# Performance work log

Hardware: AMD Instinct MI355X
Metric: run time of the kernel (lower is better)

## Reference

```python
import jax, jax.numpy as jnp
import numpy as np

MASK_FILL = -1e-07  # faithful to original (tiny negative, not -1e7)


def setup_inputs() -> dict:
    key = jax.random.key(0)
    k1, k2, k3, k4 = jax.random.split(key, 4)
    B, L1, L2, D = 64, 1024, 1024, 256
    v1 = jax.random.normal(k1, (B, L1, D), dtype=jnp.float32)
    v2 = jax.random.normal(k2, (B, L2, D), dtype=jnp.float32)
    v1_mask = jax.random.randint(k3, (B, L1), 0, 2).astype(bool)  # True = pad
    v2_mask = jax.random.randint(k4, (B, L2), 0, 2).astype(bool)
    return {"v1": v1, "v1_mask": v1_mask, "v2": v2, "v2_mask": v2_mask}


def reference(v1, v1_mask, v2, v2_mask):
    # sim: [B, L1, L2]
    sim = jnp.einsum('bld,bmd->blm', v1, v2)
    # mask rows (pad positions of v1), then softmax over L1 (dim=1)
    sim1 = jnp.where(v1_mask[:, :, None], MASK_FILL, sim)
    v2_v1_attn = jax.nn.softmax(sim1, axis=1)
    # mask columns on the already row-masked matrix, softmax over L2 (dim=2)
    sim2 = jnp.where(v2_mask[:, None, :], MASK_FILL, sim1)
    v1_v2_attn = jax.nn.softmax(sim2, axis=2)
    attended_v1 = jnp.einsum('blm,bmd->bld', v1_v2_attn, v2)  # [B, L1, D]
    attended_v2 = jnp.einsum('blm,bld->bmd', v2_v1_attn, v1)  # [B, L2, D]
    attended_v1 = jnp.where(v1_mask[:, :, None], 0.0, attended_v1)
    attended_v2 = jnp.where(v2_mask[:, :, None], 0.0, attended_v2)
    return attended_v1, attended_v2
```

## Files before the change

kernel.cpp:

```cpp
#include <hip/hip_runtime.h>
#include <hip/hip_bf16.h>
#include <hip/hip_fp16.h>
#include <stdint.h>


#define MASK_FILL -1e-07f

typedef unsigned short u16;
typedef _Float16 half8 __attribute__((ext_vector_type(8)));
typedef __attribute__((ext_vector_type(4))) float f32x4;
typedef __attribute__((ext_vector_type(4))) u16 u16x4;

#define NB 64
#define LL 1024
#define DD 256
#define BQ 128
#define HB 32
#define ELEMS ((size_t)NB * LL * DD)
#define NIT_STREAM 128

__device__ __forceinline__ u16 f16b(float f) {
    _Float16 h = (_Float16)f;
    return __builtin_bit_cast(u16, h);
}
__device__ __forceinline__ unsigned pkf16(float a, float b) {
    return (unsigned)f16b(a) | ((unsigned)f16b(b) << 16);
}

__device__ __forceinline__ void gll16(const u16* g, u16* l) {
    __builtin_amdgcn_global_load_lds(
        (const __attribute__((address_space(1))) void*)g,
        (__attribute__((address_space(3))) void*)l, 16, 0, 0);
}

__global__ __launch_bounds__(256) void prep_masks(
    const void* __restrict__ m1, const void* __restrict__ m2,
    int* __restrict__ cm1, int* __restrict__ cm2,
    int* __restrict__ qidx1, int* __restrict__ pa1, int* __restrict__ qcnt1,
    int* __restrict__ qidx2, int* __restrict__ pa2, int* __restrict__ qcnt2,
    int* __restrict__ ctr)
{
    int blk = blockIdx.x, tid = threadIdx.x;
    int msk = blk >> 6, b = blk & 63;
    const unsigned* w1 = (const unsigned*)m1;
    const unsigned* w2 = (const unsigned*)m2;
    unsigned acc = 0;
    for (int i = tid; i < 4096; i += 256) acc |= (w1[i] | w2[i]) & ~1u;
    __shared__ unsigned red[256];
    red[tid] = acc;
    __syncthreads();
    for (int o = 128; o; o >>= 1) {
        if (tid < o) red[tid] |= red[tid + o];
        __syncthreads();
    }
    int isbool = red[0] ? 1 : 0;

    const void* m = msk ? m2 : m1;
    int* cm   = msk ? cm2 : cm1;
    int* qidx = msk ? qidx2 : qidx1;
    int* pa   = msk ? pa2 : pa1;
    int* qcnt = msk ? qcnt2 : qcnt1;

    __shared__ int ps[256];
    int f[4], s = 0;
#pragma unroll
    for (int j = 0; j < 4; ++j) {
        int idx = b * LL + tid * 4 + j;
        int v = isbool ? (int)((const unsigned char*)m)[idx] : ((const int*)m)[idx];
        cm[idx] = v ? 1 : 0;
        f[j] = (v == 0) ? 1 : 0;
        s += f[j];
    }
    ps[tid] = s;
    __syncthreads();
    for (int off = 1; off < 256; off <<= 1) {
        int v = (tid >= off) ? ps[tid - off] : 0;
        __syncthreads();
        ps[tid] += v;
        __syncthreads();
    }
    int pos = (tid > 0) ? ps[tid - 1] : 0;
#pragma unroll
    for (int j = 0; j < 4; ++j) {
        pa[b * LL + tid * 4 + j] = pos;
        if (f[j]) qidx[b * LL + (pos++)] = tid * 4 + j;
    }
    if (tid == 255) qcnt[b] = ps[255];
    if (blk == 0 && tid < 8) ctr[tid] = 0;
}

__global__ __launch_bounds__(256) void prep2_kernel(
    const float* __restrict__ x1, u16* __restrict__ h1, u16* __restrict__ t1,
    const int* __restrict__ cm1, const int* __restrict__ pa1,
    const int* __restrict__ qi1, const int* __restrict__ qc1,
    const float* __restrict__ x2, u16* __restrict__ h2, u16* __restrict__ t2,
    const int* __restrict__ cm2, const int* __restrict__ pa2,
    const int* __restrict__ qi2, const int* __restrict__ qc2,
    float* __restrict__ part, float* __restrict__ out)
{
    __shared__ u16 t[64][65];
    __shared__ float ps2[16][68];
    int blk = blockIdx.x;
    int tensor = blk >> 12;
    blk &= 4095;
    const float* x = tensor ? x2 : x1;
    u16* h  = tensor ? h2 : h1;
    u16* xt = tensor ? t2 : t1;
    const int* cm = tensor ? cm2 : cm1;
    const int* pa = tensor ? pa2 : pa1;
    const int* qi = tensor ? qi2 : qi1;
    const int* qc = tensor ? qc2 : qc1;
    float* outb = out + (tensor ? ELEMS : 0);
    int b = blk >> 6, lt = (blk >> 2) & 15, dt = blk & 3;
    int l0 = lt * 64, d0 = dt * 64;
    int tid = threadIdx.x;
    int sub = tid >> 4;
    int c16 = tid & 15;
    float vpart[4] = {0.f, 0.f, 0.f, 0.f};
#pragma unroll
    for (int p = 0; p < 4; ++p) {
        int row = p * 16 + sub;
        int l = l0 + row;
        int masked = cm[b * LL + l];
        int slot = pa[b * LL + l];
        f32x4 v = *(const f32x4*)(x + ((size_t)b * LL + l) * DD + d0 + c16 * 4);
        u16x4 hv;
#pragma unroll
        for (int e = 0; e < 4; ++e) {
            hv[e] = f16b(v[e]);
            t[c16 * 4 + e][row] = hv[e];
            if (masked) vpart[e] += v[e];
        }
        if (!masked) {
            *(u16x4*)(h + ((size_t)b * LL + slot) * DD + d0 + c16 * 4) = hv;
        } else {
            f32x4 z4 = {0.f, 0.f, 0.f, 0.f};
            *(f32x4*)(outb + ((size_t)b * LL + l) * DD + d0 + c16 * 4) = z4;
        }
    }
#pragma unroll
    for (int e = 0; e < 4; ++e) ps2[sub][c16 * 4 + e] = vpart[e];
    __syncthreads();
    int first = pa[b * LL + l0];
    int cntb = qc[b];
    int nun = ((lt == 15) ? cntb : pa[b * LL + l0 + 64]) - first;
    int last = first + nun;
    int q0 = first >> 2;
    int nq = ((last + 3) >> 2) - q0;
    const int* qib = qi + b * LL;
#pragma unroll
    for (int p = 0; p < 4; ++p) {
        int d = p * 16 + sub;
        u16* xrow = xt + ((size_t)b * DD + d0 + d) * LL;
        for (int qq = c16; qq < nq; qq += 16) {
            int s0 = (q0 + qq) << 2;
            if (s0 >= first && s0 + 4 <= last) {
                u16x4 ov;
#pragma unroll
                for (int e = 0; e < 4; ++e) {
                    int col = qib[s0 + e] - l0;
                    ov[e] = t[d][col];
                }
                *(u16x4*)(xrow + s0) = ov;
            } else {
#pragma unroll
                for (int e = 0; e < 4; ++e) {
                    int sl = s0 + e;
                    if (sl >= first && sl < last) {
                        int col = qib[sl] - l0;
                        xrow[sl] = t[d][col];
                    }
                }
            }
        }
    }
    if (tid < 64) {
        float s = 0.f;
#pragma unroll
        for (int k = 0; k < 16; ++k) s += ps2[k][tid];
        part[(((size_t)tensor * NB + b) * 16 + lt) * 256 + d0 + tid] = s;
    }
}

__global__ __launch_bounds__(256) void vsum_reduce(
    const float* __restrict__ part, float* __restrict__ vsum)
{
    int blk = blockIdx.x;
    int d = threadIdx.x;
    float s = 0.f;
#pragma unroll
    for (int lt = 0; lt < 16; ++lt)
        s += part[((size_t)blk * 16 + lt) * 256 + d];
    vsum[(size_t)blk * DD + d] = s;
}

__global__ __launch_bounds__(512, 2) void flash_fused(
    const u16* __restrict__ v1h, const u16* __restrict__ v2h,
    const u16* __restrict__ v1t, const u16* __restrict__ v2t,
    const int* __restrict__ qidx1, const int* __restrict__ qcnt1,
    const int* __restrict__ qidx2, const int* __restrict__ qcnt2,
    const float* __restrict__ vsum, int* __restrict__ ctr,
    float* __restrict__ out)
{
    int strm0 = blockIdx.x & 7;
    int tid = threadIdx.x;
    int w = tid >> 6, lane = tid & 63;
    int lq = lane & 15, g = lane >> 4;

    __shared__ __align__(16) u16 khs[2][2][HB * DD];
    __shared__ __align__(16) u16 vts[2][2][HB * DD];

    const int pvcc = (g ^ (lq & 3) ^ ((lq >> 2) & 3)) * 8;

#define STAGE(BUF, KT2)                                                         \
    {                                                                           \
        int k0s = (KT2) * 64;                                                   \
        _Pragma("unroll")                                                       \
        for (int t = 0; t < 8; ++t) {                                           \
            int u = t * 8 + w;                                                  \
            int n = u & 15;                                                     \
            int hh = (u >> 4) & 1;                                              \
            if (u < 32) {                                                       \
                unsigned phys = (unsigned)n * 1024u + (unsigned)lane * 16u;     \
                unsigned key = phys >> 9;                                       \
                unsigned cl = ((phys >> 4) & 31u) ^ (key & 7u);                 \
                size_t koff = kv_base + (size_t)(k0s + hh * HB + (int)key) * DD + cl * 8; \
                gll16(kh_g + koff, &khs[BUF][hh][n * 512]);                     \
            } else {                                                            \
                unsigned dv = (unsigned)n * 16u + ((unsigned)lane >> 2);        \
                unsigned cv = ((unsigned)lane & 3u) ^ (dv & 3u) ^ ((dv >> 2) & 3u); \
                size_t voff = vt_base + (size_t)dv * LL + (unsigned)(k0s + hh * HB) + cv * 8; \
                gll16(vt_g + voff, &vts[BUF][hh][n * 512]);                     \
            }                                                                   \
        }                                                                       \
    }

    for (int ss = 0; ss < 8; ++ss) {
        int s2 = (strm0 + ss) & 7;
        for (;;) {
            __syncthreads();
            if (tid == 0) *(int*)&khs[0][0][0] = atomicAdd(&ctr[s2], 1);
            __syncthreads();
            int it = *(const int*)&khs[0][0][0];
            __syncthreads();
            if (it >= NIT_STREAM) break;
            int qt  = it & 7;
            int dir = (it >> 3) & 1;
            int b   = ((it >> 4) << 3) + s2;

            const u16 *qh_g, *kh_g, *vt_g;
            const int *qidx, *qcq, *qck;
            const float* vsp;
            float* ob;
            if (dir == 0) { qh_g=v1h; kh_g=v2h; vt_g=v2t;
                            qidx=qidx1; qcq=qcnt1; qck=qcnt2;
                            vsp = vsum + ((size_t)NB + b) * DD; ob = out; }
            else          { qh_g=v2h; kh_g=v1h; vt_g=v1t;
                            qidx=qidx2; qcq=qcnt2; qck=qcnt1;
                            vsp = vsum + (size_t)b * DD; ob = out + ELEMS; }
            int cnt_q = qcq[b];
            if (qt * BQ >= cnt_q) continue;
            int cnt_k = qck[b];
            int nkt2 = (cnt_k + 63) >> 6;

            int qslot = qt * BQ + w * 16 + lq;
            bool qvalid = qslot < cnt_q;

            const u16* qbh = qh_g + ((size_t)b * LL + qslot) * DD + g * 8;
            half8 qhf[8];
#pragma unroll
            for (int ks = 0; ks < 8; ++ks)
                qhf[ks] = *(const half8*)(const void*)(qbh + ks * 32);

            float m = MASK_FILL, z = 0.f;
            f32x4 o[16];
#pragma unroll
            for (int i2 = 0; i2 < 16; ++i2) o[i2] = (f32x4){0.f, 0.f, 0.f, 0.f};

            const size_t kv_base = (size_t)b * LL * DD;
            const size_t vt_base = (size_t)b * DD * LL;

            if (nkt2 > 0) {
                int cur = 0;
                STAGE(0, 0);
                asm volatile("s_waitcnt vmcnt(0)" ::: "memory");
                __builtin_amdgcn_s_barrier();
                __builtin_amdgcn_sched_barrier(0);

                for (int kt2 = 0; kt2 < nkt2; ++kt2) {
                    int k0 = kt2 * 64;
                    if (kt2 + 1 < nkt2) STAGE(cur ^ 1, kt2 + 1);

                    f32x4 sa[2][2];
#pragma unroll
                    for (int hh = 0; hh < 2; ++hh)
#pragma unroll
                        for (int rt = 0; rt < 2; ++rt)
                            sa[hh][rt] = (f32x4){0.f, 0.f, 0.f, 0.f};
                    __builtin_amdgcn_s_setprio(1);
#pragma unroll
                    for (int hh = 0; hh < 2; ++hh) {
#pragma unroll
                        for (int ks = 0; ks < 8; ++ks) {
                            int cidx = ((ks * 4 + g) ^ (lq & 7)) * 8;
                            half8 kh0 = *(const half8*)(const void*)&khs[cur][hh][lq * 256 + cidx];
                            half8 kh1 = *(const half8*)(const void*)&khs[cur][hh][(16 + lq) * 256 + cidx];
                            sa[hh][0] = __builtin_amdgcn_mfma_f32_16x16x32_f16(kh0, qhf[ks], sa[hh][0], 0, 0, 0);
                            sa[hh][1] = __builtin_amdgcn_mfma_f32_16x16x32_f16(kh1, qhf[ks], sa[hh][1], 0, 0, 0);
                        }
                    }
                    __builtin_amdgcn_s_setprio(0);

                    half8 vfA[8], vfB[8];
#pragma unroll
                    for (int dt = 0; dt < 8; ++dt) {
                        int d = dt * 16 + lq;
                        vfA[dt] = *(const half8*)(const void*)&vts[cur][0][d * 32 + pvcc];
                        vfB[dt] = *(const half8*)(const void*)&vts[cur][1][d * 32 + pvcc];
                    }

                    float s[16];
#pragma unroll
                    for (int hh = 0; hh < 2; ++hh)
#pragma unroll
                        for (int i2 = 0; i2 < 4; ++i2) {
                            s[hh * 8 + i2]     = sa[hh][0][i2];
                            s[hh * 8 + 4 + i2] = sa[hh][1][i2];
                        }
                    if (kt2 == nkt2 - 1) {
#pragma unroll
                        for (int hh = 0; hh < 2; ++hh) {
                            int base = k0 + hh * HB + 4 * g;
#pragma unroll
                            for (int i2 = 0; i2 < 4; ++i2) {
                                if (base + i2 >= cnt_k)      s[hh * 8 + i2]     = -1e30f;
                                if (base + 16 + i2 >= cnt_k) s[hh * 8 + 4 + i2] = -1e30f;
                            }
                        }
                    }
                    float pmax = s[0];
#pragma unroll
                    for (int i2 = 1; i2 < 16; ++i2) pmax = fmaxf(pmax, s[i2]);
                    pmax = fmaxf(pmax, __shfl_xor(pmax, 16));
                    pmax = fmaxf(pmax, __shfl_xor(pmax, 32));
                    if (__any(pmax > m)) {
                        float mnew = fmaxf(m, pmax);
                        float alpha = __expf(m - mnew);
                        z *= alpha;
#pragma unroll
                        for (int i2 = 0; i2 < 16; ++i2) o[i2] *= alpha;
                        m = mnew;
                    }
                    float p[16], psum = 0.f;
#pragma unroll
                    for (int i2 = 0; i2 < 16; ++i2) { p[i2] = __expf(s[i2] - m); psum += p[i2]; }
                    psum += __shfl_xor(psum, 16);
                    psum += __shfl_xor(psum, 32);
                    z += psum;

                    union { unsigned u[4]; half8 v; } pf[2];
                    int srcA = ((lane & 16) << 1) | lq;
                    int srcB = srcA + 16;
                    bool sel = (g >> 1) != 0;
#pragma unroll
                    for (int hh = 0; hh < 2; ++hh) {
                        unsigned pk00 = pkf16(p[hh * 8 + 0], p[hh * 8 + 1]);
                        unsigned pk01 = pkf16(p[hh * 8 + 2], p[hh * 8 + 3]);
                        unsigned pk10 = pkf16(p[hh * 8 + 4], p[hh * 8 + 5]);
                        unsigned pk11 = pkf16(p[hh * 8 + 6], p[hh * 8 + 7]);
                        unsigned a00 = (unsigned)__shfl((int)pk00, srcA);
                        unsigned a01 = (unsigned)__shfl((int)pk01, srcA);
                        unsigned a10 = (unsigned)__shfl((int)pk10, srcA);
                        unsigned a11 = (unsigned)__shfl((int)pk11, srcA);
                        unsigned b00 = (unsigned)__shfl((int)pk00, srcB);
                        unsigned b01 = (unsigned)__shfl((int)pk01, srcB);
                        unsigned b10 = (unsigned)__shfl((int)pk10, srcB);
                        unsigned b11 = (unsigned)__shfl((int)pk11, srcB);
                        pf[hh].u[0] = sel ? a10 : a00;
                        pf[hh].u[1] = sel ? a11 : a01;
                        pf[hh].u[2] = sel ? b10 : b00;
                        pf[hh].u[3] = sel ? b11 : b01;
                    }

                    __builtin_amdgcn_s_setprio(1);
#pragma unroll
                    for (int dt = 0; dt < 8; ++dt) {
                        o[dt] = __builtin_amdgcn_mfma_f32_16x16x32_f16(vfA[dt], pf[0].v, o[dt], 0, 0, 0);
                        o[dt] = __builtin_amdgcn_mfma_f32_16x16x32_f16(vfB[dt], pf[1].v, o[dt], 0, 0, 0);
                    }
#pragma unroll
                    for (int dt = 8; dt < 16; ++dt) {
                        int d = dt * 16 + lq;
                        half8 vf0 = *(const half8*)(const void*)&vts[cur][0][d * 32 + pvcc];
                        half8 vf1 = *(const half8*)(const void*)&vts[cur][1][d * 32 + pvcc];
                        o[dt] = __builtin_amdgcn_mfma_f32_16x16x32_f16(vf0, pf[0].v, o[dt], 0, 0, 0);
                        o[dt] = __builtin_amdgcn_mfma_f32_16x16x32_f16(vf1, pf[1].v, o[dt], 0, 0, 0);
                    }
                    __builtin_amdgcn_s_setprio(0);

                    if (kt2 + 1 < nkt2) {
                        asm volatile("s_waitcnt vmcnt(0)" ::: "memory");
                        __builtin_amdgcn_s_barrier();
                        __builtin_amdgcn_sched_barrier(0);
                    }
                    cur ^= 1;
                }
            }

            float wl = __expf(MASK_FILL - m);
            z += (float)(LL - cnt_k) * wl;
#pragma unroll
            for (int dt = 0; dt < 16; ++dt) {
                f32x4 vv = *(const f32x4*)(vsp + dt * 16 + 4 * g);
                o[dt] += wl * vv;
            }

            if (qvalid) {
                int qrow = qidx[b * LL + qslot];
                float zinv = 1.0f / z;
                float* orow = ob + ((size_t)b * LL + qrow) * DD + 4 * g;
#pragma unroll
                for (int dt = 0; dt < 16; ++dt) {
                    f32x4 vv = o[dt] * zinv;
                    *(f32x4*)(orow + dt * 16) = vv;
                }
            }
        }
    }
#undef STAGE
}

extern "C" void kernel_launch(void* const* d_in, const int* in_sizes, int n_in,
                              void* d_out, int out_size, void* d_ws, size_t ws_size,
                              hipStream_t stream)
{
    const float* v1      = (const float*)d_in[0];
    const void*  v1_mask = d_in[1];
    const float* v2      = (const float*)d_in[2];
    const void*  v2_mask = d_in[3];
    float* out = (float*)d_out;

    u16* v1h = (u16*)d_ws;
    u16* v2h = v1h + ELEMS;
    u16* v1t = v2h + ELEMS;
    u16* v2t = v1t + ELEMS;
    int* qidx1 = (int*)(v2t + ELEMS);
    int* qcnt1 = qidx1 + NB * LL;
    int* qidx2 = qcnt1 + NB;
    int* qcnt2 = qidx2 + NB * LL;
    int* cm1   = qcnt2 + NB;
    int* cm2   = cm1 + NB * LL;
    int* pa1   = cm2 + NB * LL;
    int* pa2   = pa1 + NB * LL;
    int* ctr   = pa2 + NB * LL;
    float* part = (float*)(ctr + 16);
    float* vsum = part + 2 * NB * 16 * 256;

    prep_masks<<<dim3(128), dim3(256), 0, stream>>>(
        v1_mask, v2_mask, cm1, cm2,
        qidx1, pa1, qcnt1, qidx2, pa2, qcnt2, ctr);

    prep2_kernel<<<dim3(2 * NB * 64), dim3(256), 0, stream>>>(
        v1, v1h, v1t, cm1, pa1, qidx1, qcnt1,
        v2, v2h, v2t, cm2, pa2, qidx2, qcnt2, part, out);
    vsum_reduce<<<dim3(2 * NB), dim3(256), 0, stream>>>(part, vsum);

    flash_fused<<<dim3(256), dim3(512), 0, stream>>>(
        v1h, v2h, v1t, v2t,
        qidx1, qcnt1, qidx2, qcnt2, vsum, ctr, out);
}
```

Before: 208.6 us.

## Shrink query tile to 64 and key tile to 32 with 4-wave blocks

Halves the query tile per work item (4 waves, 256 threads) and processes a single 32-key half-tile per iteration instead of two. The grid doubles to 512 blocks and LDS per block drops to a quarter, so more blocks can fit per CU and the persistent work queue gets finer-grained items that balance better. In exchange, each K/V tile staged into LDS is reused by fewer query rows, and there are twice as many barrier-synchronised iterations, each with less MFMA work to hide load latency behind.

```diff
diff --git a/kernel.cpp b/kernel.cpp
--- a/kernel.cpp
+++ b/kernel.cpp
@@ -14,10 +14,10 @@
 #define NB 64
 #define LL 1024
 #define DD 256
-#define BQ 128
+#define BQ 64
 #define HB 32
 #define ELEMS ((size_t)NB * LL * DD)
-#define NIT_STREAM 128
+#define NIT_STREAM 256
 
 __device__ __forceinline__ u16 f16b(float f) {
     _Float16 h = (_Float16)f;
@@ -194,7 +194,7 @@
     vsum[(size_t)blk * DD + d] = s;
 }
 
-__global__ __launch_bounds__(512, 2) void flash_fused(
+__global__ __launch_bounds__(256, 2) void flash_fused(
     const u16* __restrict__ v1h, const u16* __restrict__ v2h,
     const u16* __restrict__ v1t, const u16* __restrict__ v2t,
     const int* __restrict__ qidx1, const int* __restrict__ qcnt1,
@@ -207,30 +207,29 @@
     int w = tid >> 6, lane = tid & 63;
     int lq = lane & 15, g = lane >> 4;
 
-    __shared__ __align__(16) u16 khs[2][2][HB * DD];
-    __shared__ __align__(16) u16 vts[2][2][HB * DD];
+    __shared__ __align__(16) u16 khs[2][HB * DD];
+    __shared__ __align__(16) u16 vts[2][HB * DD];
 
     const int pvcc = (g ^ (lq & 3) ^ ((lq >> 2) & 3)) * 8;
 
-#define STAGE(BUF, KT2)                                                         \
+#define STAGE(BUF, KT)                                                          \
     {                                                                           \
-        int k0s = (KT2) * 64;                                                   \
+        int k0s = (KT) * HB;                                                    \
         _Pragma("unroll")                                                       \
         for (int t = 0; t < 8; ++t) {                                           \
-            int u = t * 8 + w;                                                  \
+            int u = t * 4 + w;                                                  \
             int n = u & 15;                                                     \
-            int hh = (u >> 4) & 1;                                              \
-            if (u < 32) {                                                       \
+            if (u < 16) {                                                       \
                 unsigned phys = (unsigned)n * 1024u + (unsigned)lane * 16u;     \
                 unsigned key = phys >> 9;                                       \
                 unsigned cl = ((phys >> 4) & 31u) ^ (key & 7u);                 \
-                size_t koff = kv_base + (size_t)(k0s + hh * HB + (int)key) * DD + cl * 8; \
-                gll16(kh_g + koff, &khs[BUF][hh][n * 512]);                     \
+                size_t koff = kv_base + (size_t)(k0s + (int)key) * DD + cl * 8; \
+                gll16(kh_g + koff, &khs[BUF][n * 512]);                         \
             } else {                                                            \
                 unsigned dv = (unsigned)n * 16u + ((unsigned)lane >> 2);        \
                 unsigned cv = ((unsigned)lane & 3u) ^ (dv & 3u) ^ ((dv >> 2) & 3u); \
-                size_t voff = vt_base + (size_t)dv * LL + (unsigned)(k0s + hh * HB) + cv * 8; \
-                gll16(vt_g + voff, &vts[BUF][hh][n * 512]);                     \
+                size_t voff = vt_base + (size_t)dv * LL + (unsigned)k0s + cv * 8;   \
+                gll16(vt_g + voff, &vts[BUF][n * 512]);                         \
             }                                                                   \
         }                                                                       \
     }
@@ -239,14 +238,14 @@
         int s2 = (strm0 + ss) & 7;
         for (;;) {
             __syncthreads();
-            if (tid == 0) *(int*)&khs[0][0][0] = atomicAdd(&ctr[s2], 1);
+            if (tid == 0) *(int*)&khs[0][0] = atomicAdd(&ctr[s2], 1);
             __syncthreads();
-            int it = *(const int*)&khs[0][0][0];
+            int it = *(const int*)&khs[0][0];
             __syncthreads();
             if (it >= NIT_STREAM) break;
-            int qt  = it & 7;
-            int dir = (it >> 3) & 1;
-            int b   = ((it >> 4) << 3) + s2;
+            int qt  = it & 15;
+            int dir = (it >> 4) & 1;
+            int b   = ((it >> 5) << 3) + s2;
 
             const u16 *qh_g, *kh_g, *vt_g;
             const int *qidx, *qcq, *qck;
@@ -261,7 +260,7 @@
             int cnt_q = qcq[b];
             if (qt * BQ >= cnt_q) continue;
             int cnt_k = qck[b];
-            int nkt2 = (cnt_k + 63) >> 6;
+            int nkt = (cnt_k + HB - 1) >> 5;
 
             int qslot = qt * BQ + w * 16 + lq;
             bool qvalid = qslot < cnt_q;
@@ -280,67 +279,51 @@
             const size_t kv_base = (size_t)b * LL * DD;
             const size_t vt_base = (size_t)b * DD * LL;
 
-            if (nkt2 > 0) {
+            if (nkt > 0) {
                 int cur = 0;
                 STAGE(0, 0);
                 asm volatile("s_waitcnt vmcnt(0)" ::: "memory");
                 __builtin_amdgcn_s_barrier();
                 __builtin_amdgcn_sched_barrier(0);
 
-                for (int kt2 = 0; kt2 < nkt2; ++kt2) {
-                    int k0 = kt2 * 64;
-                    if (kt2 + 1 < nkt2) STAGE(cur ^ 1, kt2 + 1);
-
-                    f32x4 sa[2][2];
-#pragma unroll
-                    for (int hh = 0; hh < 2; ++hh)
-#pragma unroll
-                        for (int rt = 0; rt < 2; ++rt)
-                            sa[hh][rt] = (f32x4){0.f, 0.f, 0.f, 0.f};
+                for (int kt = 0; kt < nkt; ++kt) {
+                    int k0 = kt * HB;
+                    if (kt + 1 < nkt) STAGE(cur ^ 1, kt + 1);
+
+                    f32x4 sa0 = (f32x4){0.f, 0.f, 0.f, 0.f};
+                    f32x4 sa1 = (f32x4){0.f, 0.f, 0.f, 0.f};
                     __builtin_amdgcn_s_setprio(1);
 #pragma unroll
-                    for (int hh = 0; hh < 2; ++hh) {
-#pragma unroll
-                        for (int ks = 0; ks < 8; ++ks) {
-                            int cidx = ((ks * 4 + g) ^ (lq & 7)) * 8;
-                            half8 kh0 = *(const half8*)(const void*)&khs[cur][hh][lq * 256 + cidx];
-                            half8 kh1 = *(const half8*)(const void*)&khs[cur][hh][(16 + lq) * 256 + cidx];
-                            sa[hh][0] = __builtin_amdgcn_mfma_f32_16x16x32_f16(kh0, qhf[ks], sa[hh][0], 0, 0, 0);
-                            sa[hh][1] = __builtin_amdgcn_mfma_f32_16x16x32_f16(kh1, qhf[ks], sa[hh][1], 0, 0, 0);
-                        }
+                    for (int ks = 0; ks < 8; ++ks) {
+                        int cidx = ((ks * 4 + g) ^ (lq & 7)) * 8;
+                        half8 kh0 = *(const half8*)(const void*)&khs[cur][lq * 256 + cidx];
+                        half8 kh1 = *(const half8*)(const void*)&khs[cur][(16 + lq) * 256 + cidx];
+                        sa0 = __builtin_amdgcn_mfma_f32_16x16x32_f16(kh0, qhf[ks], sa0, 0, 0, 0);
+                        sa1 = __builtin_amdgcn_mfma_f32_16x16x32_f16(kh1, qhf[ks], sa1, 0, 0, 0);
                     }
                     __builtin_amdgcn_s_setprio(0);
 
-                    half8 vfA[8], vfB[8];
+                    half8 vf[8];
 #pragma unroll
                     for (int dt = 0; dt < 8; ++dt) {
                         int d = dt * 16 + lq;
-                        vfA[dt] = *(const half8*)(const void*)&vts[cur][0][d * 32 + pvcc];
-                        vfB[dt] = *(const half8*)(const void*)&vts[cur][1][d * 32 + pvcc];
-                    }
-
-                    float s[16];
-#pragma unroll
-                    for (int hh = 0; hh < 2; ++hh)
+                        vf[dt] = *(const half8*)(const void*)&vts[cur][d * 32 + pvcc];
+                    }
+
+                    float s[8];
+#pragma unroll
+                    for (int i2 = 0; i2 < 4; ++i2) { s[i2] = sa0[i2]; s[4 + i2] = sa1[i2]; }
+                    if (kt == nkt - 1) {
+                        int base = k0 + 4 * g;
 #pragma unroll
                         for (int i2 = 0; i2 < 4; ++i2) {
-                            s[hh * 8 + i2]     = sa[hh][0][i2];
-                            s[hh * 8 + 4 + i2] = sa[hh][1][i2];
+                            if (base + i2 >= cnt_k)      s[i2]     = -1e30f;
+                            if (base + 16 + i2 >= cnt_k) s[4 + i2] = -1e30f;
                         }
-                    if (kt2 == nkt2 - 1) {
-#pragma unroll
-                        for (int hh = 0; hh < 2; ++hh) {
-                            int base = k0 + hh * HB + 4 * g;
-#pragma unroll
-                            for (int i2 = 0; i2 < 4; ++i2) {
-                                if (base + i2 >= cnt_k)      s[hh * 8 + i2]     = -1e30f;
-                                if (base + 16 + i2 >= cnt_k) s[hh * 8 + 4 + i2] = -1e30f;
-                            }
-                        }
                     }
                     float pmax = s[0];
 #pragma unroll
-                    for (int i2 = 1; i2 < 16; ++i2) pmax = fmaxf(pmax, s[i2]);
+                    for (int i2 = 1; i2 < 8; ++i2) pmax = fmaxf(pmax, s[i2]);
                     pmax = fmaxf(pmax, __shfl_xor(pmax, 16));
                     pmax = fmaxf(pmax, __shfl_xor(pmax, 32));
                     if (__any(pmax > m)) {
@@ -351,54 +334,47 @@
                         for (int i2 = 0; i2 < 16; ++i2) o[i2] *= alpha;
                         m = mnew;
                     }
-                    float p[16], psum = 0.f;
-#pragma unroll
-                    for (int i2 = 0; i2 < 16; ++i2) { p[i2] = __expf(s[i2] - m); psum += p[i2]; }
+                    float p[8], psum = 0.f;
+#pragma unroll
+                    for (int i2 = 0; i2 < 8; ++i2) { p[i2] = __expf(s[i2] - m); psum += p[i2]; }
                     psum += __shfl_xor(psum, 16);
                     psum += __shfl_xor(psum, 32);
                     z += psum;
 
-                    union { unsigned u[4]; half8 v; } pf[2];
+                    unsigned pk00 = pkf16(p[0], p[1]);
+                    unsigned pk01 = pkf16(p[2], p[3]);
+                    unsigned pk10 = pkf16(p[4], p[5]);
+                    unsigned pk11 = pkf16(p[6], p[7]);
                     int srcA = ((lane & 16) << 1) | lq;
                     int srcB = srcA + 16;
+                    unsigned a00 = (unsigned)__shfl((int)pk00, srcA);
+                    unsigned a01 = (unsigned)__shfl((int)pk01, srcA);
+                    unsigned a10 = (unsigned)__shfl((int)pk10, srcA);
+                    unsigned a11 = (unsigned)__shfl((int)pk11, srcA);
+                    unsigned b00 = (unsigned)__shfl((int)pk00, srcB);
+                    unsigned b01 = (unsigned)__shfl((int)pk01, srcB);
+                    unsigned b10 = (unsigned)__shfl((int)pk10, srcB);
+                    unsigned b11 = (unsigned)__shfl((int)pk11, srcB);
                     bool sel = (g >> 1) != 0;
-#pragma unroll
-                    for (int hh = 0; hh < 2; ++hh) {
-                        unsigned pk00 = pkf16(p[hh * 8 + 0], p[hh * 8 + 1]);
-                        unsigned pk01 = pkf16(p[hh * 8 + 2], p[hh * 8 + 3]);
-                        unsigned pk10 = pkf16(p[hh * 8 + 4], p[hh * 8 + 5]);
-                        unsigned pk11 = pkf16(p[hh * 8 + 6], p[hh * 8 + 7]);
-                        unsigned a00 = (unsigned)__shfl((int)pk00, srcA);
-                        unsigned a01 = (unsigned)__shfl((int)pk01, srcA);
-                        unsigned a10 = (unsigned)__shfl((int)pk10, srcA);
-                        unsigned a11 = (unsigned)__shfl((int)pk11, srcA);
-                        unsigned b00 = (unsigned)__shfl((int)pk00, srcB);
-                        unsigned b01 = (unsigned)__shfl((int)pk01, srcB);
-                        unsigned b10 = (unsigned)__shfl((int)pk10, srcB);
-                        unsigned b11 = (unsigned)__shfl((int)pk11, srcB);
-                        pf[hh].u[0] = sel ? a10 : a00;
-                        pf[hh].u[1] = sel ? a11 : a01;
-                        pf[hh].u[2] = sel ? b10 : b00;
-                        pf[hh].u[3] = sel ? b11 : b01;
-                    }
+                    union { unsigned u[4]; half8 v; } pf;
+                    pf.u[0] = sel ? a10 : a00;
+                    pf.u[1] = sel ? a11 : a01;
+                    pf.u[2] = sel ? b10 : b00;
+                    pf.u[3] = sel ? b11 : b01;
 
                     __builtin_amdgcn_s_setprio(1);
 #pragma unroll
-                    for (int dt = 0; dt < 8; ++dt) {
-                        o[dt] = __builtin_amdgcn_mfma_f32_16x16x32_f16(vfA[dt], pf[0].v, o[dt], 0, 0, 0);
-                        o[dt] = __builtin_amdgcn_mfma_f32_16x16x32_f16(vfB[dt], pf[1].v, o[dt], 0, 0, 0);
-                    }
+                    for (int dt = 0; dt < 8; ++dt)
+                        o[dt] = __builtin_amdgcn_mfma_f32_16x16x32_f16(vf[dt], pf.v, o[dt], 0, 0, 0);
 #pragma unroll
                     for (int dt = 8; dt < 16; ++dt) {
                         int d = dt * 16 + lq;
-                        half8 vf0 = *(const half8*)(const void*)&vts[cur][0][d * 32 + pvcc];
-                        half8 vf1 = *(const half8*)(const void*)&vts[cur][1][d * 32 + pvcc];
-                        o[dt] = __builtin_amdgcn_mfma_f32_16x16x32_f16(vf0, pf[0].v, o[dt], 0, 0, 0);
-                        o[dt] = __builtin_amdgcn_mfma_f32_16x16x32_f16(vf1, pf[1].v, o[dt], 0, 0, 0);
+                        half8 vf1 = *(const half8*)(const void*)&vts[cur][d * 32 + pvcc];
+                        o[dt] = __builtin_amdgcn_mfma_f32_16x16x32_f16(vf1, pf.v, o[dt], 0, 0, 0);
                     }
                     __builtin_amdgcn_s_setprio(0);
 
-                    if (kt2 + 1 < nkt2) {
+                    if (kt + 1 < nkt) {
                         asm volatile("s_waitcnt vmcnt(0)" ::: "memory");
                         __builtin_amdgcn_s_barrier();
                         __builtin_amdgcn_sched_barrier(0);
@@ -465,7 +441,7 @@
         v2, v2h, v2t, cm2, pa2, qidx2, qcnt2, part, out);
     vsum_reduce<<<dim3(2 * NB), dim3(256), 0, stream>>>(part, vsum);
 
-    flash_fused<<<dim3(256), dim3(512), 0, stream>>>(
+    flash_fused<<<dim3(512), dim3(256), 0, stream>>>(
         v1h, v2h, v1t, v2t,
         qidx1, qcnt1, qidx2, qcnt2, vsum, ctr, out);
 }
```

New measurement: 232.9 us. +11.7%, slower.

## Process two query fragments per wave to reuse K/V tiles across 256-row blocks

Applied to the files above, without the earlier changes.

Doubles the query block from 128 to 256 rows, so each wave holds two 16-row query fragments and reuses every K fragment and V fragment loaded from LDS for both. The work-item count per stream halves to match. This cuts LDS reads and K/V staging per query row, at the cost of roughly twice the accumulator and Q registers, which may lower occupancy or cause spills. It also adds a lazy rescale threshold (+8) on the online softmax max, which skips most rescales but allows exponentials up to e^8 before renormalising, a small fp16 overflow/precision risk.

```diff
diff --git a/kernel.cpp b/kernel.cpp
--- a/kernel.cpp
+++ b/kernel.cpp
@@ -14,10 +14,10 @@
 #define NB 64
 #define LL 1024
 #define DD 256
-#define BQ 128
+#define BQ 256
 #define HB 32
 #define ELEMS ((size_t)NB * LL * DD)
-#define NIT_STREAM 128
+#define NIT_STREAM 64
 
 __device__ __forceinline__ u16 f16b(float f) {
     _Float16 h = (_Float16)f;
@@ -244,9 +244,9 @@
             int it = *(const int*)&khs[0][0][0];
             __syncthreads();
             if (it >= NIT_STREAM) break;
-            int qt  = it & 7;
-            int dir = (it >> 3) & 1;
-            int b   = ((it >> 4) << 3) + s2;
+            int qt  = it & 3;
+            int dir = (it >> 2) & 1;
+            int b   = ((it >> 3) << 3) + s2;
 
             const u16 *qh_g, *kh_g, *vt_g;
             const int *qidx, *qcq, *qck;
@@ -263,19 +263,24 @@
             int cnt_k = qck[b];
             int nkt2 = (cnt_k + 63) >> 6;
 
-            int qslot = qt * BQ + w * 16 + lq;
-            bool qvalid = qslot < cnt_q;
-
-            const u16* qbh = qh_g + ((size_t)b * LL + qslot) * DD + g * 8;
-            half8 qhf[8];
-#pragma unroll
-            for (int ks = 0; ks < 8; ++ks)
-                qhf[ks] = *(const half8*)(const void*)(qbh + ks * 32);
-
-            float m = MASK_FILL, z = 0.f;
-            f32x4 o[16];
-#pragma unroll
-            for (int i2 = 0; i2 < 16; ++i2) o[i2] = (f32x4){0.f, 0.f, 0.f, 0.f};
+            int qs0 = qt * BQ + w * 16 + lq;
+            int qs1 = qs0 + 128;
+            const u16* qb0 = qh_g + ((size_t)b * LL + qs0) * DD + g * 8;
+            const u16* qb1 = qh_g + ((size_t)b * LL + qs1) * DD + g * 8;
+            half8 qhf[2][8];
+#pragma unroll
+            for (int ks = 0; ks < 8; ++ks) {
+                qhf[0][ks] = *(const half8*)(const void*)(qb0 + ks * 32);
+                qhf[1][ks] = *(const half8*)(const void*)(qb1 + ks * 32);
+            }
+
+            float m[2] = {MASK_FILL, MASK_FILL};
+            float z[2] = {0.f, 0.f};
+            f32x4 o[2][16];
+#pragma unroll
+            for (int qf = 0; qf < 2; ++qf)
+#pragma unroll
+                for (int i2 = 0; i2 < 16; ++i2) o[qf][i2] = (f32x4){0.f, 0.f, 0.f, 0.f};
 
             const size_t kv_base = (size_t)b * LL * DD;
             const size_t vt_base = (size_t)b * DD * LL;
@@ -291,12 +296,14 @@
                     int k0 = kt2 * 64;
                     if (kt2 + 1 < nkt2) STAGE(cur ^ 1, kt2 + 1);
 
-                    f32x4 sa[2][2];
+                    f32x4 sa[2][2][2];
 #pragma unroll
                     for (int hh = 0; hh < 2; ++hh)
 #pragma unroll
                         for (int rt = 0; rt < 2; ++rt)
-                            sa[hh][rt] = (f32x4){0.f, 0.f, 0.f, 0.f};
+#pragma unroll
+                            for (int qf = 0; qf < 2; ++qf)
+                                sa[hh][rt][qf] = (f32x4){0.f, 0.f, 0.f, 0.f};
                     __builtin_amdgcn_s_setprio(1);
 #pragma unroll
                     for (int hh = 0; hh < 2; ++hh) {
@@ -305,96 +312,90 @@
                             int cidx = ((ks * 4 + g) ^ (lq & 7)) * 8;
                             half8 kh0 = *(const half8*)(const void*)&khs[cur][hh][lq * 256 + cidx];
                             half8 kh1 = *(const half8*)(const void*)&khs[cur][hh][(16 + lq) * 256 + cidx];
-                            sa[hh][0] = __builtin_amdgcn_mfma_f32_16x16x32_f16(kh0, qhf[ks], sa[hh][0], 0, 0, 0);
-                            sa[hh][1] = __builtin_amdgcn_mfma_f32_16x16x32_f16(kh1, qhf[ks], sa[hh][1], 0, 0, 0);
+                            sa[hh][0][0] = __builtin_amdgcn_mfma_f32_16x16x32_f16(kh0, qhf[0][ks], sa[hh][0][0], 0, 0, 0);
+                            sa[hh][0][1] = __builtin_amdgcn_mfma_f32_16x16x32_f16(kh0, qhf[1][ks], sa[hh][0][1], 0, 0, 0);
+                            sa[hh][1][0] = __builtin_amdgcn_mfma_f32_16x16x32_f16(kh1, qhf[0][ks], sa[hh][1][0], 0, 0, 0);
+                            sa[hh][1][1] = __builtin_amdgcn_mfma_f32_16x16x32_f16(kh1, qhf[1][ks], sa[hh][1][1], 0, 0, 0);
                         }
                     }
                     __builtin_amdgcn_s_setprio(0);
 
-                    half8 vfA[8], vfB[8];
-#pragma unroll
-                    for (int dt = 0; dt < 8; ++dt) {
-                        int d = dt * 16 + lq;
-                        vfA[dt] = *(const half8*)(const void*)&vts[cur][0][d * 32 + pvcc];
-                        vfB[dt] = *(const half8*)(const void*)&vts[cur][1][d * 32 + pvcc];
-                    }
-
-                    float s[16];
-#pragma unroll
-                    for (int hh = 0; hh < 2; ++hh)
-#pragma unroll
-                        for (int i2 = 0; i2 < 4; ++i2) {
-                            s[hh * 8 + i2]     = sa[hh][0][i2];
-                            s[hh * 8 + 4 + i2] = sa[hh][1][i2];
-                        }
-                    if (kt2 == nkt2 - 1) {
-#pragma unroll
-                        for (int hh = 0; hh < 2; ++hh) {
-                            int base = k0 + hh * HB + 4 * g;
+                    union { unsigned u[4]; half8 v; } pf[2][2];
+#pragma unroll
+                    for (int qf = 0; qf < 2; ++qf) {
+                        float s[16];
+#pragma unroll
+                        for (int hh = 0; hh < 2; ++hh)
 #pragma unroll
                             for (int i2 = 0; i2 < 4; ++i2) {
-                                if (base + i2 >= cnt_k)      s[hh * 8 + i2]     = -1e30f;
-                                if (base + 16 + i2 >= cnt_k) s[hh * 8 + 4 + i2] = -1e30f;
+                                s[hh * 8 + i2]     = sa[hh][0][qf][i2];
+                                s[hh * 8 + 4 + i2] = sa[hh][1][qf][i2];
+                            }
+                        if (kt2 == nkt2 - 1) {
+#pragma unroll
+                            for (int hh = 0; hh < 2; ++hh) {
+                                int base = k0 + hh * HB + 4 * g;
+#pragma unroll
+                                for (int i2 = 0; i2 < 4; ++i2) {
+                                    if (base + i2 >= cnt_k)      s[hh * 8 + i2]     = -1e30f;
+                                    if (base + 16 + i2 >= cnt_k) s[hh * 8 + 4 + i2] = -1e30f;
+                                }
                             }
                         }
-                    }
-                    float pmax = s[0];
-#pragma unroll
-                    for (int i2 = 1; i2 < 16; ++i2) pmax = fmaxf(pmax, s[i2]);
-                    pmax = fmaxf(pmax, __shfl_xor(pmax, 16));
-                    pmax = fmaxf(pmax, __shfl_xor(pmax, 32));
-                    if (__any(pmax > m)) {
-                        float mnew = fmaxf(m, pmax);
-                        float alpha = __expf(m - mnew);
-                        z *= alpha;
-#pragma unroll
-                        for (int i2 = 0; i2 < 16; ++i2) o[i2] *= alpha;
-                        m = mnew;
-                    }
-                    float p[16], psum = 0.f;
-#pragma unroll
-                    for (int i2 = 0; i2 < 16; ++i2) { p[i2] = __expf(s[i2] - m); psum += p[i2]; }
-                    psum += __shfl_xor(psum, 16);
-                    psum += __shfl_xor(psum, 32);
-                    z += psum;
-
-                    union { unsigned u[4]; half8 v; } pf[2];
-                    int srcA = ((lane & 16) << 1) | lq;
-                    int srcB = srcA + 16;
-                    bool sel = (g >> 1) != 0;
-#pragma unroll
-                    for (int hh = 0; hh < 2; ++hh) {
-                        unsigned pk00 = pkf16(p[hh * 8 + 0], p[hh * 8 + 1]);
-                        unsigned pk01 = pkf16(p[hh * 8 + 2], p[hh * 8 + 3]);
-                        unsigned pk10 = pkf16(p[hh * 8 + 4], p[hh * 8 + 5]);
-                        unsigned pk11 = pkf16(p[hh * 8 + 6], p[hh * 8 + 7]);
-                        unsigned a00 = (unsigned)__shfl((int)pk00, srcA);
-                        unsigned a01 = (unsigned)__shfl((int)pk01, srcA);
-                        unsigned a10 = (unsigned)__shfl((int)pk10, srcA);
-                        unsigned a11 = (unsigned)__shfl((int)pk11, srcA);
-                        unsigned b00 = (unsigned)__shfl((int)pk00, srcB);
-                        unsigned b01 = (unsigned)__shfl((int)pk01, srcB);
-                        unsigned b10 = (unsigned)__shfl((int)pk10, srcB);
-                        unsigned b11 = (unsigned)__shfl((int)pk11, srcB);
-                        pf[hh].u[0] = sel ? a10 : a00;
-                        pf[hh].u[1] = sel ? a11 : a01;
-                        pf[hh].u[2] = sel ? b10 : b00;
-                        pf[hh].u[3] = sel ? b11 : b01;
+                        float pmax = s[0];
+#pragma unroll
+                        for (int i2 = 1; i2 < 16; ++i2) pmax = fmaxf(pmax, s[i2]);
+                        pmax = fmaxf(pmax, __shfl_xor(pmax, 16));
+                        pmax = fmaxf(pmax, __shfl_xor(pmax, 32));
+                        if (__any(pmax > m[qf] + 8.f)) {
+                            float mnew = fmaxf(m[qf], pmax);
+                            float alpha = __expf(m[qf] - mnew);
+                            z[qf] *= alpha;
+#pragma unroll
+                            for (int i2 = 0; i2 < 16; ++i2) o[qf][i2] *= alpha;
+                            m[qf] = mnew;
+                        }
+                        float p[16], psum = 0.f;
+#pragma unroll
+                        for (int i2 = 0; i2 < 16; ++i2) { p[i2] = __expf(s[i2] - m[qf]); psum += p[i2]; }
+                        psum += __shfl_xor(psum, 16);
+                        psum += __shfl_xor(psum, 32);
+                        z[qf] += psum;
+
+                        int srcA = ((lane & 16) << 1) | lq;
+                        int srcB = srcA + 16;
+                        bool sel = (g >> 1) != 0;
+#pragma unroll
+                        for (int hh = 0; hh < 2; ++hh) {
+                            unsigned pk00 = pkf16(p[hh * 8 + 0], p[hh * 8 + 1]);
+                            unsigned pk01 = pkf16(p[hh * 8 + 2], p[hh * 8 + 3]);
+                            unsigned pk10 = pkf16(p[hh * 8 + 4], p[hh * 8 + 5]);
+                            unsigned pk11 = pkf16(p[hh * 8 + 6], p[hh * 8 + 7]);
+                            unsigned a00 = (unsigned)__shfl((int)pk00, srcA);
+                            unsigned a01 = (unsigned)__shfl((int)pk01, srcA);
+                            unsigned a10 = (unsigned)__shfl((int)pk10, srcA);
+                            unsigned a11 = (unsigned)__shfl((int)pk11, srcA);
+                            unsigned b00 = (unsigned)__shfl((int)pk00, srcB);
+                            unsigned b01 = (unsigned)__shfl((int)pk01, srcB);
+                            unsigned b10 = (unsigned)__shfl((int)pk10, srcB);
+                            unsigned b11 = (unsigned)__shfl((int)pk11, srcB);
+                            pf[hh][qf].u[0] = sel ? a10 : a00;
+                            pf[hh][qf].u[1] = sel ? a11 : a01;
+                            pf[hh][qf].u[2] = sel ? b10 : b00;
+                            pf[hh][qf].u[3] = sel ? b11 : b01;
+                        }
                     }
 
                     __builtin_amdgcn_s_setprio(1);
 #pragma unroll
-                    for (int dt = 0; dt < 8; ++dt) {
-                        o[dt] = __builtin_amdgcn_mfma_f32_16x16x32_f16(vfA[dt], pf[0].v, o[dt], 0, 0, 0);
-                        o[dt] = __builtin_amdgcn_mfma_f32_16x16x32_f16(vfB[dt], pf[1].v, o[dt], 0, 0, 0);
-                    }
-#pragma unroll
-                    for (int dt = 8; dt < 16; ++dt) {
+                    for (int dt = 0; dt < 16; ++dt) {
                         int d = dt * 16 + lq;
                         half8 vf0 = *(const half8*)(const void*)&vts[cur][0][d * 32 + pvcc];
                         half8 vf1 = *(const half8*)(const void*)&vts[cur][1][d * 32 + pvcc];
-                        o[dt] = __builtin_amdgcn_mfma_f32_16x16x32_f16(vf0, pf[0].v, o[dt], 0, 0, 0);
-                        o[dt] = __builtin_amdgcn_mfma_f32_16x16x32_f16(vf1, pf[1].v, o[dt], 0, 0, 0);
+                        o[0][dt] = __builtin_amdgcn_mfma_f32_16x16x32_f16(vf0, pf[0][0].v, o[0][dt], 0, 0, 0);
+                        o[0][dt] = __builtin_amdgcn_mfma_f32_16x16x32_f16(vf1, pf[1][0].v, o[0][dt], 0, 0, 0);
+                        o[1][dt] = __builtin_amdgcn_mfma_f32_16x16x32_f16(vf0, pf[0][1].v, o[1][dt], 0, 0, 0);
+                        o[1][dt] = __builtin_amdgcn_mfma_f32_16x16x32_f16(vf1, pf[1][1].v, o[1][dt], 0, 0, 0);
                     }
                     __builtin_amdgcn_s_setprio(0);
 
@@ -407,22 +408,21 @@
                 }
             }
 
-            float wl = __expf(MASK_FILL - m);
-            z += (float)(LL - cnt_k) * wl;
-#pragma unroll
-            for (int dt = 0; dt < 16; ++dt) {
-                f32x4 vv = *(const f32x4*)(vsp + dt * 16 + 4 * g);
-                o[dt] += wl * vv;
-            }
-
-            if (qvalid) {
-                int qrow = qidx[b * LL + qslot];
-                float zinv = 1.0f / z;
-                float* orow = ob + ((size_t)b * LL + qrow) * DD + 4 * g;
-#pragma unroll
-                for (int dt = 0; dt < 16; ++dt) {
-                    f32x4 vv = o[dt] * zinv;
-                    *(f32x4*)(orow + dt * 16) = vv;
+#pragma unroll
+            for (int qf = 0; qf < 2; ++qf) {
+                int qs = qf ? (qt * BQ + 128 + w * 16 + lq) : (qt * BQ + w * 16 + lq);
+                float wl = __expf(MASK_FILL - m[qf]);
+                float zq = z[qf] + (float)(LL - cnt_k) * wl;
+                if (qs < cnt_q) {
+                    int qrow = qidx[b * LL + qs];
+                    float zinv = 1.0f / zq;
+                    float* orow = ob + ((size_t)b * LL + qrow) * DD + 4 * g;
+#pragma unroll
+                    for (int dt = 0; dt < 16; ++dt) {
+                        f32x4 vv = *(const f32x4*)(vsp + dt * 16 + 4 * g);
+                        f32x4 ov = (o[qf][dt] + wl * vv) * zinv;
+                        *(f32x4*)(orow + dt * 16) = ov;
+                    }
                 }
             }
         }
```

Result: slower. 262.8 us (+26.0%).
